# Performance work log

Measured on AMD Instinct MI355X. Metric: run time of the kernel, lower is better.

Reference implementation:

```python
import jax, jax.numpy as jnp
import numpy as np

V, D, B, K = 500000, 128, 4096, 64
EPS = 1e-5
ATT_SCALE = 15.0  # original divides attention scores by 15


def setup_inputs() -> dict:
    key = jax.random.key(0)
    k1, k2, k3, k4 = jax.random.split(key, 4)
    return {
        "node_ids": jax.random.randint(k1, (B, 3), 0, V, dtype=jnp.int64) if jax.config.read("jax_enable_x64") else jax.random.randint(k1, (B, 3), 0, V).astype(jnp.int32),
        "neighbor_ids": jax.random.randint(k2, (B, 3, K), 0, V).astype(jnp.int32),
        "neighbor_mask": jax.random.randint(k3, (B, 3, K), 0, 2).astype(jnp.int32),
        "emb": jax.random.normal(k4, (V, D), dtype=jnp.float32),
        "gamma": jnp.ones((D,), dtype=jnp.float32),
        "beta": jnp.zeros((D,), dtype=jnp.float32),
    }


def _layer_norm(x, gamma, beta):
    mu = jnp.mean(x, axis=-1, keepdims=True)
    var = jnp.mean(jnp.square(x - mu), axis=-1, keepdims=True)
    return (x - mu) * jax.lax.rsqrt(var + EPS) * gamma + beta


def reference(node_ids, neighbor_ids, neighbor_mask, emb, gamma, beta):
    node = emb[node_ids]                                   # [B,3,D]
    neigh = emb[neighbor_ids] * neighbor_mask[..., None].astype(emb.dtype)  # [B,3,K,D]
    att = jnp.einsum("btkd,btd->btk", neigh, node) / ATT_SCALE             # [B,3,K]
    att_out = jnp.einsum("btk,btkd->btd", att, neigh)                       # [B,3,D]
    return _layer_norm(node + att_out, gamma, beta)
```

## Files before the change

kernel.cpp:

```cpp
#include <hip/hip_runtime.h>

#define DD 128
#define KK 64
#define NT 256
#define NG 8
#define KPG (KK / NG)

__global__ __launch_bounds__(NT, 8) void ga_kernel(
    const int*   __restrict__ node_ids,
    const int*   __restrict__ neighbor_ids,
    const int*   __restrict__ neighbor_mask,
    const float* __restrict__ emb,
    const float* __restrict__ gamma,
    const float* __restrict__ beta,
    float*       __restrict__ out,
    int B3)
{
    __shared__ float red[NG][DD];
    __shared__ float node_lds[DD];
    __shared__ int   nid_s[KK];
    __shared__ int   msk_s[KK];

    const int blk = blockIdx.x;
    if (blk >= B3) return;
    const int t = threadIdx.x;
    const int g = t >> 5;
    const int c = t & 31;

    if (t < KK) {
        nid_s[t] = neighbor_ids[(size_t)blk * KK + t];
        msk_s[t] = neighbor_mask[(size_t)blk * KK + t];
    }

    const long long nodeid = (long long)node_ids[blk];
    const float4 nv = ((const float4*)(emb + (size_t)nodeid * DD))[c];
    if (g == 0) ((float4*)node_lds)[c] = nv;
    __syncthreads();

    float4 v[KPG];
    #pragma unroll
    for (int j = 0; j < KPG; ++j) {
        const int k = g * KPG + j;
        v[j] = make_float4(0.f, 0.f, 0.f, 0.f);
        if (msk_s[k]) {
            v[j] = ((const float4*)(emb + (size_t)nid_s[k] * DD))[c];
        }
    }

    float4 acc = make_float4(0.f, 0.f, 0.f, 0.f);
    #pragma unroll
    for (int j = 0; j < KPG; ++j) {
        float p = v[j].x * nv.x + v[j].y * nv.y + v[j].z * nv.z + v[j].w * nv.w;
        p += __shfl_xor(p, 16);
        p += __shfl_xor(p, 8);
        p += __shfl_xor(p, 4);
        p += __shfl_xor(p, 2);
        p += __shfl_xor(p, 1);
        const float att = p * (1.0f / 15.0f);
        acc.x += att * v[j].x;
        acc.y += att * v[j].y;
        acc.z += att * v[j].z;
        acc.w += att * v[j].w;
    }
    ((float4*)red[g])[c] = acc;
    __syncthreads();

    if (t < 64) {
        float x0 = node_lds[t], x1 = node_lds[t + 64];
        #pragma unroll
        for (int gg = 0; gg < NG; ++gg) {
            x0 += red[gg][t];
            x1 += red[gg][t + 64];
        }
        float s = x0 + x1;
        s += __shfl_xor(s, 32); s += __shfl_xor(s, 16); s += __shfl_xor(s, 8);
        s += __shfl_xor(s, 4);  s += __shfl_xor(s, 2);  s += __shfl_xor(s, 1);
        const float mu = s * (1.0f / 128.0f);
        const float d0 = x0 - mu, d1 = x1 - mu;
        float v2 = d0 * d0 + d1 * d1;
        v2 += __shfl_xor(v2, 32); v2 += __shfl_xor(v2, 16); v2 += __shfl_xor(v2, 8);
        v2 += __shfl_xor(v2, 4);  v2 += __shfl_xor(v2, 2);  v2 += __shfl_xor(v2, 1);
        const float rs = rsqrtf(v2 * (1.0f / 128.0f) + 1e-5f);
        const size_t ob = (size_t)blk * DD;
        out[ob + t]      = d0 * rs * gamma[t]      + beta[t];
        out[ob + t + 64] = d1 * rs * gamma[t + 64] + beta[t + 64];
    }
}

extern "C" void kernel_launch(void* const* d_in, const int* in_sizes, int n_in,
                              void* d_out, int out_size, void* d_ws, size_t ws_size,
                              hipStream_t stream) {
    const int*   node_ids      = (const int*)  d_in[0];
    const int*   neighbor_ids  = (const int*)  d_in[1];
    const int*   neighbor_mask = (const int*)  d_in[2];
    const float* emb           = (const float*)d_in[3];
    const float* gamma         = (const float*)d_in[4];
    const float* beta          = (const float*)d_in[5];
    float*       out           = (float*)d_out;

    const int B3 = in_sizes[0];

    ga_kernel<<<B3, NT, 0, stream>>>(node_ids, neighbor_ids, neighbor_mask,
                                     emb, gamma, beta, out, B3);
}
```

Measured before the change: 39.97 us.

## Map one full wavefront per neighbor with scalar index loads, dropping LDS staging

The block grows from 256 to 512 threads. Each 64-lane wavefront now handles 8 neighbors, loading one float2 per lane per row, where before a 32-lane half-wave handled 8 neighbors with float4 loads. Neighbor ids and masks are read straight from global memory as wave-uniform scalar values through readfirstlane, which removes the LDS staging arrays and the first barrier. In exchange, each lane issues twice as many, narrower gather loads, the dot product needs one more shuffle stage, and the launch bound halves occupancy per block.

After: 59.43 us. 48.7% more time.

```diff
diff --git a/kernel.cpp b/kernel.cpp
--- a/kernel.cpp
+++ b/kernel.cpp
@@ -2,11 +2,11 @@
 
 #define DD 128
 #define KK 64
-#define NT 256
-#define NG 8
-#define KPG (KK / NG)
+#define NT 512
+#define NW 8
+#define KPW (KK / NW)
 
-__global__ __launch_bounds__(NT, 8) void ga_kernel(
+__global__ __launch_bounds__(NT, 4) void ga_kernel(
     const int*   __restrict__ node_ids,
     const int*   __restrict__ neighbor_ids,
     const int*   __restrict__ neighbor_mask,
@@ -16,41 +16,37 @@
     float*       __restrict__ out,
     int B3)
 {
-    __shared__ float red[NG][DD];
+    __shared__ float red[NW][DD];
     __shared__ float node_lds[DD];
-    __shared__ int   nid_s[KK];
-    __shared__ int   msk_s[KK];
 
     const int blk = blockIdx.x;
     if (blk >= B3) return;
     const int t = threadIdx.x;
-    const int g = t >> 5;
-    const int c = t & 31;
-
-    if (t < KK) {
-        nid_s[t] = neighbor_ids[(size_t)blk * KK + t];
-        msk_s[t] = neighbor_mask[(size_t)blk * KK + t];
-    }
+    const int l = t & 63;
+    const int w = __builtin_amdgcn_readfirstlane(t >> 6);
 
     const long long nodeid = (long long)node_ids[blk];
-    const float4 nv = ((const float4*)(emb + (size_t)nodeid * DD))[c];
-    if (g == 0) ((float4*)node_lds)[c] = nv;
-    __syncthreads();
+    const float2 nv = ((const float2*)(emb + (size_t)nodeid * DD))[l];
+    if (w == 0) ((float2*)node_lds)[l] = nv;
 
-    float4 v[KPG];
+    const int kbase = blk * KK + w * KPW;
+
+    float2 v[KPW];
     #pragma unroll
-    for (int j = 0; j < KPG; ++j) {
-        const int k = g * KPG + j;
-        v[j] = make_float4(0.f, 0.f, 0.f, 0.f);
-        if (msk_s[k]) {
-            v[j] = ((const float4*)(emb + (size_t)nid_s[k] * DD))[c];
+    for (int j = 0; j < KPW; ++j) {
+        const int m   = __builtin_amdgcn_readfirstlane(neighbor_mask[kbase + j]);
+        v[j] = make_float2(0.f, 0.f);
+        if (m) {
+            const int idx = __builtin_amdgcn_readfirstlane(neighbor_ids[kbase + j]);
+            v[j] = ((const float2*)(emb + (size_t)idx * DD))[l];
         }
     }
 
-    float4 acc = make_float4(0.f, 0.f, 0.f, 0.f);
+    float2 acc = make_float2(0.f, 0.f);
     #pragma unroll
-    for (int j = 0; j < KPG; ++j) {
-        float p = v[j].x * nv.x + v[j].y * nv.y + v[j].z * nv.z + v[j].w * nv.w;
+    for (int j = 0; j < KPW; ++j) {
+        float p = v[j].x * nv.x + v[j].y * nv.y;
+        p += __shfl_xor(p, 32);
         p += __shfl_xor(p, 16);
         p += __shfl_xor(p, 8);
         p += __shfl_xor(p, 4);
@@ -59,16 +55,14 @@
         const float att = p * (1.0f / 15.0f);
         acc.x += att * v[j].x;
         acc.y += att * v[j].y;
-        acc.z += att * v[j].z;
-        acc.w += att * v[j].w;
     }
-    ((float4*)red[g])[c] = acc;
+    ((float2*)red[w])[l] = acc;
     __syncthreads();
 
     if (t < 64) {
         float x0 = node_lds[t], x1 = node_lds[t + 64];
         #pragma unroll
-        for (int gg = 0; gg < NG; ++gg) {
+        for (int gg = 0; gg < NW; ++gg) {
             x0 += red[gg][t];
             x1 += red[gg][t + 64];
         }
```
